# Kernel optimization log

Hardware: AMD Instinct MI355X
Metric: run time of the kernel (lower is better)

## Reference

```python
import jax, jax.numpy as jnp
import numpy as np

B, E, K, S, D, H, C = 8192, 8, 2, 32, 3072, 256, 100  # batch, experts, fix_points, img size, flat dim, hidden, classes


def setup_inputs() -> dict:
    key = jax.random.key(0)
    ks = jax.random.split(key, 6)
    return {
        "x": jax.random.normal(ks[0], (B, 3, S, S), jnp.float32),
        "coeffs_t": jax.random.uniform(ks[1], (K,), jnp.float32),
        "router_w": jax.random.normal(ks[2], (K, D, E), jnp.float32) * 0.02,
        "router_b": jnp.zeros((K, E), jnp.float32),
        "w1": jax.random.normal(ks[3], (E, K, D, H), jnp.float32) * 0.02,
        "b1": jnp.zeros((E, K, H), jnp.float32),
        "w2": jax.random.normal(ks[4], (E, K, H, C), jnp.float32) * 0.02,
        "b2": jnp.zeros((E, K, C), jnp.float32),
    }


def reference(x, coeffs_t, router_w, router_b, w1, b1, w2, b2):
    xf = x.reshape(x.shape[0], -1)  # [B, D]
    # Curve parameter blend: W = sum_k coeffs_t[k] * W_k (CurveParameter semantics)
    Wr = jnp.einsum('k,kde->de', coeffs_t, router_w)
    br = jnp.einsum('k,ke->e', coeffs_t, router_b)
    # Router: top-1 expert index per sample
    idx = jnp.argmax(xf @ Wr + br, axis=-1)  # [B] int
    # Blended expert weights
    W1 = jnp.einsum('k,ekdh->edh', coeffs_t, w1)
    B1 = jnp.einsum('k,ekh->eh', coeffs_t, b1)
    W2 = jnp.einsum('k,ekhc->ehc', coeffs_t, w2)
    B2 = jnp.einsum('k,ekc->ec', coeffs_t, b2)
    # Expert MLP (computed for all experts with static shapes, then top-1 gather;
    # identical math to torch's boolean-mask dispatch/scatter)
    h = jax.nn.gelu(jnp.einsum('bd,edh->beh', xf, W1) + B1, approximate=False)  # [B,E,H]
    o = jnp.einsum('beh,ehc->bec', h, W2) + B2  # [B,E,C]
    return jnp.take_along_axis(o, idx[:, None, None], axis=1)[:, 0, :]  # [B,C]
```

## Files before the change

kernel.cpp:

```cpp
#include <hip/hip_runtime.h>
#include <math.h>

#define B_  8192
#define E_  8
#define D_  3072
#define H_  256
#define C_  100
#define DH_ (D_*H_)
#define HC_ (H_*C_)
#define KS_ 8
#define KSEG_ (D_/KS_)
#define RKS_ 8
#define RSEG_ (D_/RKS_)
#define NTMAX_ 136

typedef __attribute__((ext_vector_type(4))) float  f32x4;
typedef __attribute__((ext_vector_type(8))) __bf16 bf16x8;
typedef __attribute__((ext_vector_type(8))) unsigned short ush8;
typedef __attribute__((ext_vector_type(4))) unsigned short ush4;

__device__ inline unsigned short bf16_rne(float f) {
    unsigned u = __builtin_bit_cast(unsigned, f);
    unsigned r = (u + 0x7FFFu + ((u >> 16) & 1u)) >> 16;
    return (unsigned short)r;
}
__device__ inline float bf16_f(unsigned short h) {
    unsigned u = ((unsigned)h) << 16;
    return __builtin_bit_cast(float, u);
}

__global__ void blend4_k(const float4* __restrict__ in, float4* __restrict__ out,
                         const float* __restrict__ coeffs, int inner4, int total4) {
    float c0 = coeffs[0], c1 = coeffs[1];
    for (int i = blockIdx.x * blockDim.x + threadIdx.x; i < total4;
         i += gridDim.x * blockDim.x) {
        int e = i / inner4;
        int r = i - e * inner4;
        const float4* p = in + (size_t)e * 2 * inner4 + r;
        float4 a = p[0];
        float4 b = p[inner4];
        float4 o;
        o.x = c0 * a.x + c1 * b.x;
        o.y = c0 * a.y + c1 * b.y;
        o.z = c0 * a.z + c1 * b.z;
        o.w = c0 * a.w + c1 * b.w;
        out[i] = o;
    }
}

#define TP_ 136
__global__ __launch_bounds__(256) void blendw1t_k(
        const float* __restrict__ w1, unsigned short* __restrict__ Whi,
        unsigned short* __restrict__ Wlo, const float* __restrict__ coeffs) {
    __shared__ unsigned short thi[64 * TP_];
    __shared__ unsigned short tlo[64 * TP_];
    float c0 = coeffs[0], c1 = coeffs[1];
    int t = threadIdx.x;
    int e = blockIdx.z, h0 = blockIdx.y * 64, d0 = blockIdx.x * 128;
    int h = t & 63, dl = t >> 6;
    const float* pa = w1 + ((size_t)(e * 2 + 0) * D_ + d0) * H_ + h0 + h;
    const float* pb = w1 + ((size_t)(e * 2 + 1) * D_ + d0) * H_ + h0 + h;
    for (int it = 0; it < 32; it++) {
        int d = it * 4 + dl;
        float v = c0 * pa[(size_t)d * H_] + c1 * pb[(size_t)d * H_];
        unsigned short hi = bf16_rne(v);
        thi[h * TP_ + d] = hi;
        tlo[h * TP_ + d] = bf16_rne(v - bf16_f(hi));
    }
    __syncthreads();
    #pragma unroll
    for (int it = 0; it < 4; it++) {
        int i = t + it * 256;
        int hh = i >> 4, d8 = (i & 15) * 8;
        size_t g = (size_t)(e * H_ + h0 + hh) * D_ + d0 + d8;
        *(ush8*)(Whi + g) = *(const ush8*)&thi[hh * TP_ + d8];
        *(ush8*)(Wlo + g) = *(const ush8*)&tlo[hh * TP_ + d8];
    }
}

__global__ __launch_bounds__(256) void blendw2t_k(
        const float* __restrict__ w2, unsigned short* __restrict__ W2thi,
        unsigned short* __restrict__ W2tlo, const float* __restrict__ coeffs) {
    float c0 = coeffs[0], c1 = coeffs[1];
    int c = blockIdx.x, e = blockIdx.y, k = threadIdx.x;
    float v = c0 * w2[((size_t)(e * 2 + 0) * H_ + k) * C_ + c]
            + c1 * w2[((size_t)(e * 2 + 1) * H_ + k) * C_ + c];
    unsigned short hi = bf16_rne(v);
    W2thi[(size_t)(e * C_ + c) * H_ + k] = hi;
    W2tlo[(size_t)(e * C_ + c) * H_ + k] = bf16_rne(v - bf16_f(hi));
}

__global__ __launch_bounds__(256) void blendrw_k(
        const float* __restrict__ rw, double* __restrict__ wsd,
        const float* __restrict__ coeffs) {
    double c0 = (double)coeffs[0], c1 = (double)coeffs[1];
    int d = blockIdx.x * 256 + threadIdx.x;
    #pragma unroll
    for (int ee = 0; ee < 8; ee++)
        wsd[(size_t)d * 8 + ee] = c0 * (double)rw[(size_t)d * 8 + ee]
                                + c1 * (double)rw[(size_t)(D_ + d) * 8 + ee];
}

__global__ __launch_bounds__(64) void router_v2_k(
        const float* __restrict__ x, const double* __restrict__ wsd,
        double* __restrict__ lpart) {
    __shared__ float  xs[64][33];
    __shared__ double wls[32][8];
    int lane = threadIdx.x;
    int row0 = blockIdx.x * 64;
    int kbase = blockIdx.y * RSEG_;

    double acc[8] = {0, 0, 0, 0, 0, 0, 0, 0};

    for (int kb = 0; kb < RSEG_; kb += 32) {
        #pragma unroll
        for (int it = 0; it < 8; it++) {
            int i = lane + it * 64;
            int r = i >> 3, c4 = i & 7;
            *(float4*)&xs[r][c4 * 4] =
                *(const float4*)(x + (size_t)(row0 + r) * D_ + kbase + kb + c4 * 4);
        }
        #pragma unroll
        for (int it = 0; it < 4; it++) {
            int i = lane + it * 64;
            int k = i >> 3, ee = i & 7;
            wls[k][ee] = wsd[(size_t)(kbase + kb + k) * 8 + ee];
        }
        __syncthreads();
        #pragma unroll
        for (int kk = 0; kk < 32; kk++) {
            double xv = (double)xs[lane][kk];
            double2 w01 = *(const double2*)&wls[kk][0];
            double2 w23 = *(const double2*)&wls[kk][2];
            double2 w45 = *(const double2*)&wls[kk][4];
            double2 w67 = *(const double2*)&wls[kk][6];
            acc[0] = fma(xv, w01.x, acc[0]);
            acc[1] = fma(xv, w01.y, acc[1]);
            acc[2] = fma(xv, w23.x, acc[2]);
            acc[3] = fma(xv, w23.y, acc[3]);
            acc[4] = fma(xv, w45.x, acc[4]);
            acc[5] = fma(xv, w45.y, acc[5]);
            acc[6] = fma(xv, w67.x, acc[6]);
            acc[7] = fma(xv, w67.y, acc[7]);
        }
        __syncthreads();
    }
    size_t base = ((size_t)blockIdx.y * B_ + row0 + lane) * 8;
    #pragma unroll
    for (int ee = 0; ee < 8; ee++) lpart[base + ee] = acc[ee];
}

__global__ __launch_bounds__(256) void argmax_k(
        const double* __restrict__ lpart, const float* __restrict__ rb,
        const float* __restrict__ coeffs, int* __restrict__ idx,
        int* __restrict__ cnt) {
    __shared__ int scnt[8];
    int t = threadIdx.x;
    if (t < 8) scnt[t] = 0;
    __syncthreads();
    int b = blockIdx.x * 256 + t;
    double c0 = (double)coeffs[0], c1 = (double)coeffs[1];
    double best = -1e300;
    int bi = 0;
    #pragma unroll
    for (int e = 0; e < 8; e++) {
        double l = c0 * (double)rb[e] + c1 * (double)rb[8 + e];
        #pragma unroll
        for (int s2 = 0; s2 < RKS_; s2++)
            l += lpart[((size_t)s2 * B_ + b) * 8 + e];
        if (l > best) { best = l; bi = e; }
    }
    idx[b] = bi;
    atomicAdd(&scnt[bi], 1);
    __syncthreads();
    if (t < 8 && scnt[t] > 0) atomicAdd(&cnt[t], scnt[t]);
}

__global__ void offsets_k(const int* __restrict__ cnt, int* __restrict__ off,
                          int* __restrict__ cursor, int* __restrict__ tmap,
                          int* __restrict__ ntl) {
    if (threadIdx.x == 0) {
        int s = 0;
        for (int e = 0; e < E_; e++) { off[e] = s; cursor[e] = s; s += cnt[e]; }
        int nt = 0;
        for (int e = 0; e < E_; e++)
            for (int t0 = 0; t0 < cnt[e]; t0 += 64)
                tmap[nt++] = (e << 16) | t0;
        ntl[0] = nt;
    }
}

__global__ void scatter_k(const int* __restrict__ idx, int* __restrict__ cursor,
                          int* __restrict__ order) {
    int b = blockIdx.x * blockDim.x + threadIdx.x;
    if (b < B_) {
        int e = idx[b];
        int pos = atomicAdd(&cursor[e], 1);
        order[pos] = (e << 16) | b;
    }
}

template<int MODE>
__global__ __launch_bounds__(256, 3) void gemm1_t(
        const float* __restrict__ x, const unsigned short* __restrict__ Whi,
        const unsigned short* __restrict__ Wlo, const int* __restrict__ order,
        const int* __restrict__ cnt, const int* __restrict__ off,
        const int* __restrict__ tmap, const int* __restrict__ ntl,
        float* __restrict__ dst) {
    int tid = blockIdx.y;
    if (tid >= ntl[0]) return;
    int tm = tmap[tid];
    int e = tm >> 16, tile0 = tm & 0xFFFF;
    int ce = cnt[e];
    int s = blockIdx.x;

    __shared__ int rows[64];
    __shared__ unsigned short xs_hi[64 * 40];
    __shared__ unsigned short xs_lo[64 * 40];
    __shared__ unsigned short ws_hi[256 * 40];
    __shared__ unsigned short ws_lo[256 * 40];

    int t = threadIdx.x;
    if (t < 64) {
        int i = tile0 + t;
        rows[t] = (i < ce) ? (order[off[e] + i] & 0xFFFF) : -1;
    }
    __syncthreads();
    int xrow0 = rows[0];

    int lane = t & 63, w = t >> 6;
    int lr = lane & 15, quad = lane >> 4;
    int kbase = s * KSEG_;

    f32x4 acc[4][4];
    #pragma unroll
    for (int mt = 0; mt < 4; mt++)
        #pragma unroll
        for (int nt = 0; nt < 4; nt++)
            acc[mt][nt] = (f32x4){0.f, 0.f, 0.f, 0.f};

    for (int kb = 0; kb < KSEG_; kb += 32) {
        #pragma unroll
        for (int it = 0; it < 2; it++) {
            int i = t + it * 256;
            int rr = i >> 3, sg = i & 7;
            int row = rows[rr];
            if (row < 0) row = xrow0;
            float4 v = *(const float4*)(x + (size_t)row * D_ + kbase + kb + sg * 4);
            unsigned short h4[4], l4[4];
            float vv[4] = {v.x, v.y, v.z, v.w};
            #pragma unroll
            for (int j = 0; j < 4; j++) {
                unsigned short hi = bf16_rne(vv[j]);
                h4[j] = hi;
                l4[j] = bf16_rne(vv[j] - bf16_f(hi));
            }
            *(ush4*)&xs_hi[rr * 40 + sg * 4] = *(const ush4*)h4;
            *(ush4*)&xs_lo[rr * 40 + sg * 4] = *(const ush4*)l4;
        }
        #pragma unroll
        for (int it = 0; it < 4; it++) {
            int i = t + it * 256;
            int col = i >> 2, ch = i & 3;
            size_t g = (size_t)(e * H_ + col) * D_ + kbase + kb + ch * 8;
            *(ush8*)&ws_hi[col * 40 + ch * 8] = *(const ush8*)(Whi + g);
            *(ush8*)&ws_lo[col * 40 + ch * 8] = *(const ush8*)(Wlo + g);
        }
        __syncthreads();

        bf16x8 ah[4], al[4], bh[4], bl[4];
        #pragma unroll
        for (int mt = 0; mt < 4; mt++) {
            ah[mt] = __builtin_bit_cast(bf16x8, *(const ush8*)&xs_hi[(mt * 16 + lr) * 40 + quad * 8]);
            al[mt] = __builtin_bit_cast(bf16x8, *(const ush8*)&xs_lo[(mt * 16 + lr) * 40 + quad * 8]);
        }
        #pragma unroll
        for (int nt = 0; nt < 4; nt++) {
            int col = w * 64 + nt * 16 + lr;
            bh[nt] = __builtin_bit_cast(bf16x8, *(const ush8*)&ws_hi[col * 40 + quad * 8]);
            bl[nt] = __builtin_bit_cast(bf16x8, *(const ush8*)&ws_lo[col * 40 + quad * 8]);
        }
        #pragma unroll
        for (int mt = 0; mt < 4; mt++)
            #pragma unroll
            for (int nt = 0; nt < 4; nt++) {
                acc[mt][nt] = __builtin_amdgcn_mfma_f32_16x16x32_bf16(ah[mt], bh[nt], acc[mt][nt], 0, 0, 0);
                acc[mt][nt] = __builtin_amdgcn_mfma_f32_16x16x32_bf16(al[mt], bh[nt], acc[mt][nt], 0, 0, 0);
                acc[mt][nt] = __builtin_amdgcn_mfma_f32_16x16x32_bf16(ah[mt], bl[nt], acc[mt][nt], 0, 0, 0);
                acc[mt][nt] = __builtin_amdgcn_mfma_f32_16x16x32_bf16(al[mt], bl[nt], acc[mt][nt], 0, 0, 0);
            }
        __syncthreads();
    }

    size_t p0 = (size_t)off[e] + tile0;
    if (MODE == 1) {
        float* dp = dst + ((size_t)s * B_ + p0) * H_;
        #pragma unroll
        for (int mt = 0; mt < 4; mt++) {
            int rl = mt * 16 + quad * 4;
            #pragma unroll
            for (int nt = 0; nt < 4; nt++) {
                int col = w * 64 + nt * 16 + lr;
                #pragma unroll
                for (int rg = 0; rg < 4; rg++) {
                    if (tile0 + rl + rg < ce)
                        dp[(size_t)(rl + rg) * H_ + col] = acc[mt][nt][rg];
                }
            }
        }
    } else {
        #pragma unroll
        for (int mt = 0; mt < 4; mt++) {
            int rl = mt * 16 + quad * 4;
            #pragma unroll
            for (int nt = 0; nt < 4; nt++) {
                int col = w * 64 + nt * 16 + lr;
                #pragma unroll
                for (int rg = 0; rg < 4; rg++) {
                    if (tile0 + rl + rg < ce)
                        atomicAdd(&dst[(p0 + rl + rg) * H_ + col], acc[mt][nt][rg]);
                }
            }
        }
    }
}

__global__ __launch_bounds__(256) void reduce_gelu_k(
        float* __restrict__ hpart, const float* __restrict__ B1b,
        const int* __restrict__ order) {
    int gid = blockIdx.x * 256 + threadIdx.x;
    int p = gid >> 6, c4 = (gid & 63) * 4;
    int e = order[p] >> 16;
    size_t o = (size_t)p * H_ + c4;
    float4 a = *(const float4*)(hpart + o);
    #pragma unroll
    for (int s2 = 1; s2 < KS_; s2++) {
        float4 b = *(const float4*)(hpart + (size_t)s2 * B_ * H_ + o);
        a.x += b.x; a.y += b.y; a.z += b.z; a.w += b.w;
    }
    const float4 bb = *(const float4*)(B1b + e * H_ + c4);
    float pre[4] = {a.x + bb.x, a.y + bb.y, a.z + bb.z, a.w + bb.w};
    float4 og;
    og.x = 0.5f * pre[0] * (1.0f + erff(pre[0] * 0.70710678118654752440f));
    og.y = 0.5f * pre[1] * (1.0f + erff(pre[1] * 0.70710678118654752440f));
    og.z = 0.5f * pre[2] * (1.0f + erff(pre[2] * 0.70710678118654752440f));
    og.w = 0.5f * pre[3] * (1.0f + erff(pre[3] * 0.70710678118654752440f));
    *(float4*)(hpart + o) = og;
}

__global__ __launch_bounds__(256) void bias_gelu_k(
        float* __restrict__ hws, const float* __restrict__ B1b,
        const int* __restrict__ order) {
    int gid = blockIdx.x * 256 + threadIdx.x;
    int p = gid >> 6, c4 = (gid & 63) * 4;
    int e = order[p] >> 16;
    float4 v = *(const float4*)(hws + (size_t)p * H_ + c4);
    const float4 bb = *(const float4*)(B1b + e * H_ + c4);
    float pre[4] = {v.x + bb.x, v.y + bb.y, v.z + bb.z, v.w + bb.w};
    float4 o;
    o.x = 0.5f * pre[0] * (1.0f + erff(pre[0] * 0.70710678118654752440f));
    o.y = 0.5f * pre[1] * (1.0f + erff(pre[1] * 0.70710678118654752440f));
    o.z = 0.5f * pre[2] * (1.0f + erff(pre[2] * 0.70710678118654752440f));
    o.w = 0.5f * pre[3] * (1.0f + erff(pre[3] * 0.70710678118654752440f));
    *(float4*)(hws + (size_t)p * H_ + c4) = o;
}

__global__ __launch_bounds__(256) void gemm2_k(
        const float* __restrict__ hws,
        const unsigned short* __restrict__ W2thi, const unsigned short* __restrict__ W2tlo,
        const float* __restrict__ B2b, const int* __restrict__ order,
        const int* __restrict__ cnt, const int* __restrict__ off,
        const int* __restrict__ tmap, const int* __restrict__ ntl,
        float* __restrict__ out) {
    int tid = blockIdx.x;
    if (tid >= ntl[0]) return;
    int tm = tmap[tid];
    int e = tm >> 16, tile0 = tm & 0xFFFF;
    int ce = cnt[e];

    __shared__ int rows[64];
    int t = threadIdx.x;
    if (t < 64) {
        int i = tile0 + t;
        rows[t] = (i < ce) ? (order[off[e] + i] & 0xFFFF) : -1;
    }
    __syncthreads();

    int lane = t & 63, w = t >> 6;
    int m = lane & 15, q = lane >> 4;
    int lr = w * 16 + m;
    int p = off[e] + tile0 + ((tile0 + lr < ce) ? lr : 0);

    f32x4 acc[7];
    #pragma unroll
    for (int nt = 0; nt < 7; nt++) acc[nt] = (f32x4){0.f, 0.f, 0.f, 0.f};

    const unsigned short* w2h = W2thi + (size_t)e * C_ * H_;
    const unsigned short* w2l = W2tlo + (size_t)e * C_ * H_;

    #pragma unroll
    for (int s = 0; s < 8; s++) {
        float4 v0 = *(const float4*)(hws + (size_t)p * H_ + s * 32 + q * 8);
        float4 v1 = *(const float4*)(hws + (size_t)p * H_ + s * 32 + q * 8 + 4);
        float f[8] = {v0.x, v0.y, v0.z, v0.w, v1.x, v1.y, v1.z, v1.w};
        unsigned short hh[8], lo[8];
        #pragma unroll
        for (int j = 0; j < 8; j++) {
            unsigned short hi = bf16_rne(f[j]);
            hh[j] = hi;
            lo[j] = bf16_rne(f[j] - bf16_f(hi));
        }
        bf16x8 ah = __builtin_bit_cast(bf16x8, *(const ush8*)hh);
        bf16x8 al = __builtin_bit_cast(bf16x8, *(const ush8*)lo);
        #pragma unroll
        for (int nt = 0; nt < 7; nt++) {
            size_t bo = (size_t)(nt * 16 + m) * H_ + s * 32 + q * 8;
            bf16x8 bh = __builtin_bit_cast(bf16x8, *(const ush8*)(w2h + bo));
            bf16x8 bl = __builtin_bit_cast(bf16x8, *(const ush8*)(w2l + bo));
            acc[nt] = __builtin_amdgcn_mfma_f32_16x16x32_bf16(ah, bh, acc[nt], 0, 0, 0);
            acc[nt] = __builtin_amdgcn_mfma_f32_16x16x32_bf16(al, bh, acc[nt], 0, 0, 0);
            acc[nt] = __builtin_amdgcn_mfma_f32_16x16x32_bf16(ah, bl, acc[nt], 0, 0, 0);
            acc[nt] = __builtin_amdgcn_mfma_f32_16x16x32_bf16(al, bl, acc[nt], 0, 0, 0);
        }
    }

    #pragma unroll
    for (int nt = 0; nt < 7; nt++) {
        int c = nt * 16 + m;
        if (c >= C_) continue;
        float bias = B2b[e * C_ + c];
        #pragma unroll
        for (int i = 0; i < 4; i++) {
            int lrow = w * 16 + q * 4 + i;
            if (tile0 + lrow < ce)
                out[(size_t)rows[lrow] * C_ + c] = acc[nt][i] + bias;
        }
    }
}

extern "C" void kernel_launch(void* const* d_in, const int* in_sizes, int n_in,
                              void* d_out, int out_size, void* d_ws, size_t ws_size,
                              hipStream_t stream) {
    const float* x        = (const float*)d_in[0];
    const float* coeffs   = (const float*)d_in[1];
    const float* router_w = (const float*)d_in[2];
    const float* router_b = (const float*)d_in[3];
    const float* w1       = (const float*)d_in[4];
    const float* b1       = (const float*)d_in[5];
    const float* w2       = (const float*)d_in[6];
    const float* b2       = (const float*)d_in[7];
    float* out = (float*)d_out;

    unsigned short* Whi   = (unsigned short*)d_ws;
    unsigned short* Wlo   = Whi + (size_t)E_ * DH_;
    unsigned short* W2thi = Wlo + (size_t)E_ * DH_;
    unsigned short* W2tlo = W2thi + (size_t)E_ * C_ * H_;
    float* B1b  = (float*)(W2tlo + (size_t)E_ * C_ * H_);
    float* B2b  = B1b + (size_t)E_ * H_;
    int* order  = (int*)(B2b + E_ * C_);
    int* cnt    = order + B_;
    int* off    = cnt + E_;
    int* cursor = off + E_;
    int* tmap   = cursor + E_;
    int* ntl    = tmap + NTMAX_;
    float* hws  = (float*)(ntl + 4);
    double* lpart = (double*)hws;
    double* wsd   = (double*)((char*)hws + (size_t)RKS_ * B_ * 8 * 8);
    int*    idx   = (int*)((char*)hws + (5u << 20));

    size_t prefix_bytes = (size_t)((char*)hws - (char*)d_ws);
    int use_part = (ws_size >= prefix_bytes + (size_t)KS_ * B_ * H_ * sizeof(float) + 256) ? 1 : 0;

    hipMemsetAsync(cnt, 0, 3 * E_ * sizeof(int), stream);

    blendw1t_k<<<dim3(D_ / 128, H_ / 64, E_), 256, 0, stream>>>(w1, Whi, Wlo, coeffs);
    blendw2t_k<<<dim3(C_, E_), 256, 0, stream>>>(w2, W2thi, W2tlo, coeffs);
    blend4_k<<<dim3(2), 256, 0, stream>>>((const float4*)b1, (float4*)B1b,
                                          coeffs, H_ / 4, E_ * (H_ / 4));
    blend4_k<<<dim3(1), 256, 0, stream>>>((const float4*)b2, (float4*)B2b,
                                          coeffs, C_ / 4, E_ * (C_ / 4));
    blendrw_k<<<dim3(D_ / 256), 256, 0, stream>>>(router_w, wsd, coeffs);

    router_v2_k<<<dim3(B_ / 64, RKS_), 64, 0, stream>>>(x, wsd, lpart);
    argmax_k<<<dim3(B_ / 256), 256, 0, stream>>>(lpart, router_b, coeffs, idx, cnt);
    offsets_k<<<1, 64, 0, stream>>>(cnt, off, cursor, tmap, ntl);
    scatter_k<<<dim3(B_ / 256), 256, 0, stream>>>(idx, cursor, order);

    if (use_part) {
        gemm1_t<1><<<dim3(KS_, NTMAX_), 256, 0, stream>>>(x, Whi, Wlo, order, cnt,
                                                          off, tmap, ntl, hws);
        reduce_gelu_k<<<dim3(B_ * H_ / 4 / 256), 256, 0, stream>>>(hws, B1b, order);
    } else {
        hipMemsetAsync(hws, 0, (size_t)B_ * H_ * sizeof(float), stream);
        gemm1_t<0><<<dim3(KS_, NTMAX_), 256, 0, stream>>>(x, Whi, Wlo, order, cnt,
                                                          off, tmap, ntl, hws);
        bias_gelu_k<<<dim3(B_ * H_ / 4 / 256), 256, 0, stream>>>(hws, B1b, order);
    }
    gemm2_k<<<dim3(NTMAX_), 256, 0, stream>>>(hws, W2thi, W2tlo, B2b, order,
                                              cnt, off, tmap, ntl, out);
}
```

Measured before the change: 366.3 us.

## Register-prefetch next K-slice in gemm1, raise MFMA priority, merge small blend kernels

The gemm1 main loop now loads the next 32-wide K slice of x and the split-bf16 weights into registers right after the barrier, so global loads overlap the MFMA work of the current slice. The x/weight addresses are precomputed once outside the loop. s_setprio is raised around the MFMA block. Separately, the three small bias/router blend launches are merged into one kernel to cut launch overhead. Register pressure rises from the prefetch buffers, which may reduce occupancy.

```diff
diff --git a/kernel.cpp b/kernel.cpp
--- a/kernel.cpp
+++ b/kernel.cpp
@@ -29,22 +29,48 @@
     return __builtin_bit_cast(float, u);
 }
 
-__global__ void blend4_k(const float4* __restrict__ in, float4* __restrict__ out,
-                         const float* __restrict__ coeffs, int inner4, int total4) {
+#define MISC_B1_ (E_*H_/4)
+#define MISC_B2_ (E_*C_/4)
+#define MISC_TOT_ (MISC_B1_ + MISC_B2_ + D_)
+__global__ __launch_bounds__(256) void blend_misc_k(
+        const float* __restrict__ b1, const float* __restrict__ b2,
+        const float* __restrict__ rw, float* __restrict__ B1b,
+        float* __restrict__ B2b, double* __restrict__ wsd,
+        const float* __restrict__ coeffs) {
+    int gid = blockIdx.x * 256 + threadIdx.x;
     float c0 = coeffs[0], c1 = coeffs[1];
-    for (int i = blockIdx.x * blockDim.x + threadIdx.x; i < total4;
-         i += gridDim.x * blockDim.x) {
-        int e = i / inner4;
-        int r = i - e * inner4;
-        const float4* p = in + (size_t)e * 2 * inner4 + r;
-        float4 a = p[0];
-        float4 b = p[inner4];
+    if (gid < MISC_B1_) {
+        const float4* p = (const float4*)b1;
+        int e = gid / (H_ / 4), r = gid - e * (H_ / 4);
+        float4 a = p[(e * 2 + 0) * (H_ / 4) + r];
+        float4 bq = p[(e * 2 + 1) * (H_ / 4) + r];
         float4 o;
-        o.x = c0 * a.x + c1 * b.x;
-        o.y = c0 * a.y + c1 * b.y;
-        o.z = c0 * a.z + c1 * b.z;
-        o.w = c0 * a.w + c1 * b.w;
-        out[i] = o;
+        o.x = c0 * a.x + c1 * bq.x;
+        o.y = c0 * a.y + c1 * bq.y;
+        o.z = c0 * a.z + c1 * bq.z;
+        o.w = c0 * a.w + c1 * bq.w;
+        ((float4*)B1b)[gid] = o;
+    } else if (gid < MISC_B1_ + MISC_B2_) {
+        int g2 = gid - MISC_B1_;
+        const float4* p = (const float4*)b2;
+        int e = g2 / (C_ / 4), r = g2 - e * (C_ / 4);
+        float4 a = p[(e * 2 + 0) * (C_ / 4) + r];
+        float4 bq = p[(e * 2 + 1) * (C_ / 4) + r];
+        float4 o;
+        o.x = c0 * a.x + c1 * bq.x;
+        o.y = c0 * a.y + c1 * bq.y;
+        o.z = c0 * a.z + c1 * bq.z;
+        o.w = c0 * a.w + c1 * bq.w;
+        ((float4*)B2b)[g2] = o;
+    } else {
+        int d = gid - (MISC_B1_ + MISC_B2_);
+        if (d < D_) {
+            double c0d = (double)c0, c1d = (double)c1;
+            #pragma unroll
+            for (int ee = 0; ee < 8; ee++)
+                wsd[(size_t)d * 8 + ee] = c0d * (double)rw[(size_t)d * 8 + ee]
+                                        + c1d * (double)rw[(size_t)(D_ + d) * 8 + ee];
+        }
     }
 }
 
@@ -90,17 +116,6 @@
     W2tlo[(size_t)(e * C_ + c) * H_ + k] = bf16_rne(v - bf16_f(hi));
 }
 
-__global__ __launch_bounds__(256) void blendrw_k(
-        const float* __restrict__ rw, double* __restrict__ wsd,
-        const float* __restrict__ coeffs) {
-    double c0 = (double)coeffs[0], c1 = (double)coeffs[1];
-    int d = blockIdx.x * 256 + threadIdx.x;
-    #pragma unroll
-    for (int ee = 0; ee < 8; ee++)
-        wsd[(size_t)d * 8 + ee] = c0 * (double)rw[(size_t)d * 8 + ee]
-                                + c1 * (double)rw[(size_t)(D_ + d) * 8 + ee];
-}
-
 __global__ __launch_bounds__(64) void router_v2_k(
         const float* __restrict__ x, const double* __restrict__ wsd,
         double* __restrict__ lpart) {
@@ -232,6 +247,23 @@
     int lr = lane & 15, quad = lane >> 4;
     int kbase = s * KSEG_;
 
+    int sg = t & 7;
+    int rr0 = t >> 3, rr1 = (t + 256) >> 3;
+    int rowa = rows[rr0]; if (rowa < 0) rowa = xrow0;
+    int rowb = rows[rr1]; if (rowb < 0) rowb = xrow0;
+    const float* xp0 = x + (size_t)rowa * D_ + kbase + sg * 4;
+    const float* xp1 = x + (size_t)rowb * D_ + kbase + sg * 4;
+    int xo0 = rr0 * 40 + sg * 4, xo1 = rr1 * 40 + sg * 4;
+    size_t wgo[4];
+    int wdo[4];
+    #pragma unroll
+    for (int it = 0; it < 4; it++) {
+        int i = t + it * 256;
+        int col = i >> 2, ch = i & 3;
+        wgo[it] = (size_t)(e * H_ + col) * D_ + kbase + ch * 8;
+        wdo[it] = col * 40 + ch * 8;
+    }
+
     f32x4 acc[4][4];
     #pragma unroll
     for (int mt = 0; mt < 4; mt++)
@@ -239,34 +271,56 @@
         for (int nt = 0; nt < 4; nt++)
             acc[mt][nt] = (f32x4){0.f, 0.f, 0.f, 0.f};
 
+    float4 px0 = *(const float4*)xp0;
+    float4 px1 = *(const float4*)xp1;
+    ush8 pwh[4], pwl[4];
+    #pragma unroll
+    for (int it = 0; it < 4; it++) {
+        pwh[it] = *(const ush8*)(Whi + wgo[it]);
+        pwl[it] = *(const ush8*)(Wlo + wgo[it]);
+    }
+
     for (int kb = 0; kb < KSEG_; kb += 32) {
-        #pragma unroll
-        for (int it = 0; it < 2; it++) {
-            int i = t + it * 256;
-            int rr = i >> 3, sg = i & 7;
-            int row = rows[rr];
-            if (row < 0) row = xrow0;
-            float4 v = *(const float4*)(x + (size_t)row * D_ + kbase + kb + sg * 4);
+        {
+            float vv[4] = {px0.x, px0.y, px0.z, px0.w};
             unsigned short h4[4], l4[4];
-            float vv[4] = {v.x, v.y, v.z, v.w};
             #pragma unroll
             for (int j = 0; j < 4; j++) {
                 unsigned short hi = bf16_rne(vv[j]);
                 h4[j] = hi;
                 l4[j] = bf16_rne(vv[j] - bf16_f(hi));
             }
-            *(ush4*)&xs_hi[rr * 40 + sg * 4] = *(const ush4*)h4;
-            *(ush4*)&xs_lo[rr * 40 + sg * 4] = *(const ush4*)l4;
+            *(ush4*)&xs_hi[xo0] = *(const ush4*)h4;
+            *(ush4*)&xs_lo[xo0] = *(const ush4*)l4;
+        }
+        {
+            float vv[4] = {px1.x, px1.y, px1.z, px1.w};
+            unsigned short h4[4], l4[4];
+            #pragma unroll
+            for (int j = 0; j < 4; j++) {
+                unsigned short hi = bf16_rne(vv[j]);
+                h4[j] = hi;
+                l4[j] = bf16_rne(vv[j] - bf16_f(hi));
+            }
+            *(ush4*)&xs_hi[xo1] = *(const ush4*)h4;
+            *(ush4*)&xs_lo[xo1] = *(const ush4*)l4;
         }
         #pragma unroll
         for (int it = 0; it < 4; it++) {
-            int i = t + it * 256;
-            int col = i >> 2, ch = i & 3;
-            size_t g = (size_t)(e * H_ + col) * D_ + kbase + kb + ch * 8;
-            *(ush8*)&ws_hi[col * 40 + ch * 8] = *(const ush8*)(Whi + g);
-            *(ush8*)&ws_lo[col * 40 + ch * 8] = *(const ush8*)(Wlo + g);
+            *(ush8*)&ws_hi[wdo[it]] = pwh[it];
+            *(ush8*)&ws_lo[wdo[it]] = pwl[it];
         }
         __syncthreads();
+
+        if (kb + 32 < KSEG_) {
+            px0 = *(const float4*)(xp0 + kb + 32);
+            px1 = *(const float4*)(xp1 + kb + 32);
+            #pragma unroll
+            for (int it = 0; it < 4; it++) {
+                pwh[it] = *(const ush8*)(Whi + wgo[it] + kb + 32);
+                pwl[it] = *(const ush8*)(Wlo + wgo[it] + kb + 32);
+            }
+        }
 
         bf16x8 ah[4], al[4], bh[4], bl[4];
         #pragma unroll
@@ -280,6 +334,7 @@
             bh[nt] = __builtin_bit_cast(bf16x8, *(const ush8*)&ws_hi[col * 40 + quad * 8]);
             bl[nt] = __builtin_bit_cast(bf16x8, *(const ush8*)&ws_lo[col * 40 + quad * 8]);
         }
+        __builtin_amdgcn_s_setprio(1);
         #pragma unroll
         for (int mt = 0; mt < 4; mt++)
             #pragma unroll
@@ -289,6 +344,7 @@
                 acc[mt][nt] = __builtin_amdgcn_mfma_f32_16x16x32_bf16(ah[mt], bl[nt], acc[mt][nt], 0, 0, 0);
                 acc[mt][nt] = __builtin_amdgcn_mfma_f32_16x16x32_bf16(al[mt], bl[nt], acc[mt][nt], 0, 0, 0);
             }
+        __builtin_amdgcn_s_setprio(0);
         __syncthreads();
     }
 
@@ -475,11 +531,8 @@
 
     blendw1t_k<<<dim3(D_ / 128, H_ / 64, E_), 256, 0, stream>>>(w1, Whi, Wlo, coeffs);
     blendw2t_k<<<dim3(C_, E_), 256, 0, stream>>>(w2, W2thi, W2tlo, coeffs);
-    blend4_k<<<dim3(2), 256, 0, stream>>>((const float4*)b1, (float4*)B1b,
-                                          coeffs, H_ / 4, E_ * (H_ / 4));
-    blend4_k<<<dim3(1), 256, 0, stream>>>((const float4*)b2, (float4*)B2b,
-                                          coeffs, C_ / 4, E_ * (C_ / 4));
-    blendrw_k<<<dim3(D_ / 256), 256, 0, stream>>>(router_w, wsd, coeffs);
+    blend_misc_k<<<dim3((MISC_TOT_ + 255) / 256), 256, 0, stream>>>(
+        b1, b2, router_w, B1b, B2b, wsd, coeffs);
 
     router_v2_k<<<dim3(B_ / 64, RKS_), 64, 0, stream>>>(x, wsd, lpart);
     argmax_k<<<dim3(B_ / 256), 256, 0, stream>>>(lpart, router_b, coeffs, idx, cnt);
```

New measurement: 500.2 us. 36.5% more time.
